# Kernel optimization log

Hardware: AMD Instinct MI355X
Metric: run time of the kernel (lower is better)

Reference implementation:

```python
import jax, jax.numpy as jnp
import numpy as np

T, B, I, H, LBL = 200, 1024, 128, 128, 4


def setup_inputs() -> dict:
    key = jax.random.key(0)
    ks = jax.random.split(key, 14)
    si = 1.0 / np.sqrt(I)
    sh = 1.0 / np.sqrt(H)
    inputs = jax.random.normal(ks[0], (T, B, I), jnp.float32)
    lengths = jnp.maximum(jax.random.randint(ks[1], (B,), 1, T + 1), LBL).astype(jnp.int32)
    return {
        "inputs": inputs,
        "lengths": lengths,
        "Wih_g": jax.random.normal(ks[2], (3 * H, I), jnp.float32) * si,
        "Whh_g": jax.random.normal(ks[3], (3 * H, H), jnp.float32) * sh,
        "bih_g": jax.random.normal(ks[4], (3 * H,), jnp.float32) * sh,
        "bhh_g": jax.random.normal(ks[5], (3 * H,), jnp.float32) * sh,
        "Wih_l": jax.random.normal(ks[6], (3 * H, I), jnp.float32) * si,
        "Whh_l": jax.random.normal(ks[7], (3 * H, H), jnp.float32) * sh,
        "bih_l": jax.random.normal(ks[8], (3 * H,), jnp.float32) * sh,
        "bhh_l": jax.random.normal(ks[9], (3 * H,), jnp.float32) * sh,
        "A1": jax.random.normal(ks[10], (H, H), jnp.float32) * sh,
        "A2": jax.random.normal(ks[11], (H, H), jnp.float32) * sh,
        "v1": jax.random.normal(ks[12], (1, H), jnp.float32) * sh,
        "label_len": LBL,
    }


def gru(x, Wih, Whh, bih, bhh):
    # x: [T, B, I] time-major. PyTorch GRU cell semantics.
    Bq, Hq = x.shape[1], Whh.shape[1]
    gi_all = jnp.einsum('tbi,gi->tbg', x, Wih) + bih  # precompute input projections [T,B,3H]
    def step(h, gi):
        gh = h @ Whh.T + bhh
        ir, iz, inn = jnp.split(gi, 3, axis=-1)
        hr, hz, hn = jnp.split(gh, 3, axis=-1)
        r = jax.nn.sigmoid(ir + hr)
        z = jax.nn.sigmoid(iz + hz)
        n = jnp.tanh(inn + r * hn)
        h = (1.0 - z) * n + z * h
        return h, h
    h0 = jnp.zeros((Bq, Hq), x.dtype)
    _, hs = jax.lax.scan(step, h0, gi_all)
    return hs  # [T, B, H]


def reference(inputs, lengths, Wih_g, Whh_g, bih_g, bhh_g,
              Wih_l, Whh_l, bih_l, bhh_l, A1, A2, v1, label_len):
    h_g = gru(inputs, Wih_g, Whh_g, bih_g, bhh_g)  # [T,B,H]
    h_l = gru(inputs, Wih_l, Whh_l, bih_l, bhh_l)  # [T,B,H]
    # attention score per step s: v1(sigmoid(A1 h_l + A2 h_g)), query-independent
    pre = jax.nn.sigmoid(jnp.einsum('tbh,gh->tbg', h_l, A1) +
                         jnp.einsum('tbh,gh->tbg', h_g, A2))
    scores = jnp.einsum('tbg,og->tbo', pre, v1)  # [T,B,1]
    # per-t output = cumsum_{s<=t}(score*h_l) + h_g[t]
    out = jnp.cumsum(scores * h_l, axis=0) + h_g  # [T,B,H]
    out_b = jnp.transpose(out, (1, 0, 2))  # [B,T,H]
    # gather last label_len timesteps of each sequence: h[b,k] = out[L_b-label_len+k, b]
    idx = lengths[:, None].astype(jnp.int32) - label_len + jnp.arange(label_len, dtype=jnp.int32)[None, :]
    idx = jnp.clip(idx, 0, out_b.shape[1] - 1)  # [B, label_len]
    h = jnp.take_along_axis(out_b, idx[:, :, None], axis=1)  # [B, label_len, H]
    return h
```

## Files before the change

### kernel.cpp

```cpp
#include <hip/hip_runtime.h>
#include <stdint.h>


typedef __attribute__((ext_vector_type(8))) short short8;
typedef __attribute__((ext_vector_type(4))) float float4v;

#define LDS_BARRIER() asm volatile("s_waitcnt lgkmcnt(0)\n\ts_barrier" ::: "memory")

__device__ inline float bf2f(unsigned short u){
  union { unsigned int i; float f; } v; v.i = ((unsigned int)u) << 16; return v.f;
}
__device__ inline unsigned short f2bf(float f){
  union { float f; unsigned int i; } v; v.f = f;
  unsigned int x = v.i;
  return (unsigned short)((x + 0x7fffu + ((x >> 16) & 1u)) >> 16);
}
__device__ inline unsigned int pack2(float a, float b){
  return (unsigned int)f2bf(a) | ((unsigned int)f2bf(b) << 16);
}
__device__ inline float sigm(float x){ return __builtin_amdgcn_rcpf(1.0f + __expf(-x)); }
__device__ inline float tanhfast(float x){ return 1.0f - 2.0f * __builtin_amdgcn_rcpf(__expf(2.0f * x) + 1.0f); }

__global__ void k_prep(unsigned short* hl_slot, unsigned short* hg_slot, float* cum)
{
  int i = blockIdx.x * blockDim.x + threadIdx.x;
  hl_slot[i] = 0;
  hg_slot[i] = 0;
  cum[i] = 0.0f;
}

__global__ __launch_bounds__(512, 2) void k_scan(
    const float* __restrict__ x,
    const float* __restrict__ Wih_g, const float* __restrict__ Whh_g,
    const float* __restrict__ bih_g, const float* __restrict__ bhh_g,
    const float* __restrict__ Wih_l, const float* __restrict__ Whh_l,
    const float* __restrict__ bih_l, const float* __restrict__ bhh_l,
    unsigned short* __restrict__ hl_seq, unsigned short* __restrict__ hg_seq,
    int tc, int t0)
{
  __shared__ __align__(16) unsigned short hbuf[2][16][136];
  __shared__ __align__(16) unsigned short xbuf[2][16][136];
  int tid = threadIdx.x;
  int w = tid >> 6, L = tid & 63, l15 = L & 15, q = L >> 4;
  int gru = blockIdx.x & 1;
  int b0 = (blockIdx.x >> 1) * 16;
  const float* Wih = gru ? Wih_l : Wih_g;
  const float* Whh = gru ? Whh_l : Whh_g;
  const float* bih = gru ? bih_l : bih_g;
  const float* bhh = gru ? bhh_l : bhh_g;
  unsigned short* myseq = gru ? hl_seq : hg_seq;

  int col = w * 16 + l15;

  short8 Wi[3][4], Wh[3][4];
  #pragma unroll
  for (int G = 0; G < 3; G++) {
    int row = G * 128 + col;
    #pragma unroll
    for (int kf = 0; kf < 4; kf++) {
      const float4* p0 = (const float4*)(Wih + (size_t)row * 128 + kf * 32 + q * 8);
      const float4* p1 = (const float4*)(Whh + (size_t)row * 128 + kf * 32 + q * 8);
      float4 a0 = p0[0], a1 = p0[1], b0f = p1[0], b1f = p1[1];
      short8 si, sh;
      si[0]=(short)f2bf(a0.x); si[1]=(short)f2bf(a0.y); si[2]=(short)f2bf(a0.z); si[3]=(short)f2bf(a0.w);
      si[4]=(short)f2bf(a1.x); si[5]=(short)f2bf(a1.y); si[6]=(short)f2bf(a1.z); si[7]=(short)f2bf(a1.w);
      sh[0]=(short)f2bf(b0f.x); sh[1]=(short)f2bf(b0f.y); sh[2]=(short)f2bf(b0f.z); sh[3]=(short)f2bf(b0f.w);
      sh[4]=(short)f2bf(b1f.x); sh[5]=(short)f2bf(b1f.y); sh[6]=(short)f2bf(b1f.z); sh[7]=(short)f2bf(b1f.w);
      Wi[G][kf] = si; Wh[G][kf] = sh;
    }
  }
  float br  = bih[col]       + bhh[col];
  float bz  = bih[128 + col] + bhh[128 + col];
  float bin = bih[256 + col];
  float bnh = bhh[256 + col];

  float hold[4];
  #pragma unroll
  for (int r = 0; r < 4; r++) {
    int m = q * 4 + r;
    unsigned short u = myseq[((size_t)(tc - 1) * 1024 + b0 + m) * 128 + col];
    hold[r] = bf2f(u);
    hbuf[0][m][col] = u;
  }
  {
    float4 x0 = ((const float4*)(x + ((size_t)t0 * 1024 + b0) * 128))[tid];
    int row = tid >> 5, c4 = (tid & 31) * 4;
    *(uint2*)&xbuf[0][row][c4] = make_uint2(pack2(x0.x, x0.y), pack2(x0.z, x0.w));
  }
  int tn = t0 + (tc > 1 ? 1 : 0);
  float4 xr = ((const float4*)(x + ((size_t)tn * 1024 + b0) * 128))[tid];
  __syncthreads();

  int p = 0;
  for (int s = 0; s < tc; s++) {
    short8 Ah[4], Ax[4];
    #pragma unroll
    for (int kf = 0; kf < 4; kf++) {
      Ah[kf] = *(const short8*)&hbuf[p][l15][kf * 32 + q * 8];
      Ax[kf] = *(const short8*)&xbuf[p][l15][kf * 32 + q * 8];
    }
    if (s + 1 < tc) {
      int row = tid >> 5, c4 = (tid & 31) * 4;
      *(uint2*)&xbuf[1 - p][row][c4] = make_uint2(pack2(xr.x, xr.y), pack2(xr.z, xr.w));
    }
    {
      int t2 = t0 + (s + 2 < tc ? s + 2 : tc - 1);
      xr = ((const float4*)(x + ((size_t)t2 * 1024 + b0) * 128))[tid];
    }
    float4v arz0 = (float4v){0.f,0.f,0.f,0.f};
    float4v arz1 = (float4v){0.f,0.f,0.f,0.f};
    float4v anx  = (float4v){0.f,0.f,0.f,0.f};
    float4v anh  = (float4v){0.f,0.f,0.f,0.f};
    #pragma unroll
    for (int kf = 0; kf < 4; kf++) arz0 = __builtin_amdgcn_mfma_f32_16x16x32_bf16(Ax[kf], Wi[0][kf], arz0, 0,0,0);
    #pragma unroll
    for (int kf = 0; kf < 4; kf++) arz1 = __builtin_amdgcn_mfma_f32_16x16x32_bf16(Ax[kf], Wi[1][kf], arz1, 0,0,0);
    #pragma unroll
    for (int kf = 0; kf < 4; kf++) anx  = __builtin_amdgcn_mfma_f32_16x16x32_bf16(Ax[kf], Wi[2][kf], anx,  0,0,0);
    #pragma unroll
    for (int kf = 0; kf < 4; kf++) anh  = __builtin_amdgcn_mfma_f32_16x16x32_bf16(Ah[kf], Wh[2][kf], anh,  0,0,0);
    #pragma unroll
    for (int kf = 0; kf < 4; kf++) arz0 = __builtin_amdgcn_mfma_f32_16x16x32_bf16(Ah[kf], Wh[0][kf], arz0, 0,0,0);
    #pragma unroll
    for (int kf = 0; kf < 4; kf++) arz1 = __builtin_amdgcn_mfma_f32_16x16x32_bf16(Ah[kf], Wh[1][kf], arz1, 0,0,0);

    #pragma unroll
    for (int r = 0; r < 4; r++) {
      int m = q * 4 + r;
      float rr = sigm(arz0[r] + br);
      float zz = sigm(arz1[r] + bz);
      float nn = tanhfast(anx[r] + bin + rr * (anh[r] + bnh));
      float hn = nn + zz * (hold[r] - nn);
      hold[r] = hn;
      unsigned short hu = f2bf(hn);
      hbuf[1 - p][m][col] = hu;
      myseq[((size_t)s * 1024 + b0 + m) * 128 + col] = hu;
    }
    p ^= 1;
    LDS_BARRIER();
  }
}

__global__ __launch_bounds__(256) void k_score(const unsigned short* __restrict__ hl_seq,
                                               const unsigned short* __restrict__ hg_seq,
                                               const float* __restrict__ A1,
                                               const float* __restrict__ A2,
                                               const float* __restrict__ v1,
                                               float* __restrict__ score, int tc)
{
  __shared__ __align__(16) unsigned short M1[128][136];
  __shared__ __align__(16) unsigned short M2[128][136];
  int tid = threadIdx.x;
  int w = tid >> 6, L = tid & 63;
  int l15 = L & 15, q = L >> 4;
  int s = blockIdx.x;

  #pragma unroll
  for (int it = 0; it < 16; it++) {
    int f4 = it * 256 + tid;
    float4 a = ((const float4*)A1)[f4];
    float4 b = ((const float4*)A2)[f4];
    *(uint2*)&M1[f4 >> 5][(f4 & 31) * 4] = make_uint2(pack2(a.x, a.y), pack2(a.z, a.w));
    *(uint2*)&M2[f4 >> 5][(f4 & 31) * 4] = make_uint2(pack2(b.x, b.y), pack2(b.z, b.w));
  }
  __syncthreads();

  float v1v[8];
  #pragma unroll
  for (int nt = 0; nt < 8; nt++) v1v[nt] = v1[nt * 16 + l15];

  short8 Fl[4], Fg[4], Pl[4], Pg[4];
  {
    size_t base = ((size_t)s * 1024 + (size_t)w * 16 + l15) * 128;
    #pragma unroll
    for (int kf = 0; kf < 4; kf++) {
      Fl[kf] = *(const short8*)(hl_seq + base + kf * 32 + q * 8);
      Fg[kf] = *(const short8*)(hg_seq + base + kf * 32 + q * 8);
    }
  }
  for (int it = 0; it < 16; it++) {
    int b0 = (it * 4 + w) * 16;
    if (it + 1 < 16) {
      size_t base = ((size_t)s * 1024 + (size_t)((it + 1) * 4 + w) * 16 + l15) * 128;
      #pragma unroll
      for (int kf = 0; kf < 4; kf++) {
        Pl[kf] = *(const short8*)(hl_seq + base + kf * 32 + q * 8);
        Pg[kf] = *(const short8*)(hg_seq + base + kf * 32 + q * 8);
      }
    }
    float4v acc[8];
    #pragma unroll
    for (int nt = 0; nt < 8; nt++) {
      float4v a = (float4v){0.f, 0.f, 0.f, 0.f};
      #pragma unroll
      for (int kf = 0; kf < 4; kf++)
        a = __builtin_amdgcn_mfma_f32_16x16x32_bf16(
            Fl[kf], *(const short8*)&M1[nt * 16 + l15][kf * 32 + q * 8], a, 0, 0, 0);
      #pragma unroll
      for (int kf = 0; kf < 4; kf++)
        a = __builtin_amdgcn_mfma_f32_16x16x32_bf16(
            Fg[kf], *(const short8*)&M2[nt * 16 + l15][kf * 32 + q * 8], a, 0, 0, 0);
      acc[nt] = a;
    }
    float p4[4];
    #pragma unroll
    for (int r = 0; r < 4; r++) {
      float sum = 0.f;
      #pragma unroll
      for (int nt = 0; nt < 8; nt++) sum += v1v[nt] * sigm(acc[nt][r]);
      sum += __shfl_xor(sum, 1, 16);
      sum += __shfl_xor(sum, 2, 16);
      sum += __shfl_xor(sum, 4, 16);
      sum += __shfl_xor(sum, 8, 16);
      p4[r] = sum;
    }
    if (l15 == 0) {
      #pragma unroll
      for (int r = 0; r < 4; r++)
        score[(size_t)(b0 + q * 4 + r) * tc + s] = p4[r];
    }
    #pragma unroll
    for (int kf = 0; kf < 4; kf++) { Fl[kf] = Pl[kf]; Fg[kf] = Pg[kf]; }
  }
}

__global__ __launch_bounds__(256) void k_cum(const float* __restrict__ score,
                                             const unsigned short* __restrict__ hl_seq,
                                             const unsigned short* __restrict__ hg_seq,
                                             const int* __restrict__ lengths,
                                             float* __restrict__ cum,
                                             float* __restrict__ out, int tc, int t0)
{
  __shared__ __align__(16) unsigned short hlL[100 * 256];
  __shared__ float scL[2][100];
  int tid = threadIdx.x;
  int b2 = tid >> 7, j = tid & 127;
  int b0 = blockIdx.x * 2;
  int b = b0 + b2;
  int base = b2 * 128 + j;

  float c = cum[(size_t)b * 128 + j];
  int cap0 = lengths[b] - 4;

  float hgv[4];
  #pragma unroll
  for (int d = 0; d < 4; d++) {
    int sl = cap0 + d - t0;
    hgv[d] = (sl >= 0 && sl < tc) ? bf2f(hg_seq[((size_t)sl * 1024 + b) * 128 + j]) : 0.f;
  }

  for (int seg = 0; seg < tc; seg += 100) {
    int len = (tc - seg < 100) ? (tc - seg) : 100;
    __syncthreads();
    for (int f8 = tid; f8 < len * 32; f8 += 256) {
      int sl = f8 >> 5, r8 = f8 & 31;
      *(short8*)&hlL[(size_t)f8 * 8] =
          *(const short8*)(hl_seq + ((size_t)(seg + sl) * 1024 + b0) * 128 + r8 * 8);
    }
    for (int i = tid; i < 2 * len; i += 256) {
      int bb = (i >= len) ? 1 : 0;
      int sl = i - bb * len;
      scL[bb][sl] = score[(size_t)(b0 + bb) * tc + seg + sl];
    }
    __syncthreads();

    int sl = 0;
    for (; sl + 5 <= len; sl += 5) {
      float h[5], sc[5];
      #pragma unroll
      for (int k = 0; k < 5; k++) {
        h[k] = bf2f(hlL[(size_t)(sl + k) * 256 + base]);
        sc[k] = scL[b2][sl + k];
      }
      #pragma unroll
      for (int k = 0; k < 5; k++) {
        c += sc[k] * h[k];
        int d = (t0 + seg + sl + k) - cap0;
        if ((unsigned)d < 4u)
          out[((size_t)b * 4 + d) * 128 + j] = c + hgv[d];
      }
    }
    for (; sl < len; sl++) {
      c += scL[b2][sl] * bf2f(hlL[(size_t)sl * 256 + base]);
      int d = (t0 + seg + sl) - cap0;
      if ((unsigned)d < 4u)
        out[((size_t)b * 4 + d) * 128 + j] = c + hgv[d];
    }
  }
  cum[(size_t)b * 128 + j] = c;
}

extern "C" void kernel_launch(void* const* d_in, const int* in_sizes, int n_in,
                              void* d_out, int out_size, void* d_ws, size_t ws_size,
                              hipStream_t stream)
{
  const float* x     = (const float*)d_in[0];
  const int* lengths = (const int*)d_in[1];
  const float* Wih_g = (const float*)d_in[2];
  const float* Whh_g = (const float*)d_in[3];
  const float* bih_g = (const float*)d_in[4];
  const float* bhh_g = (const float*)d_in[5];
  const float* Wih_l = (const float*)d_in[6];
  const float* Whh_l = (const float*)d_in[7];
  const float* bih_l = (const float*)d_in[8];
  const float* bhh_l = (const float*)d_in[9];
  const float* A1    = (const float*)d_in[10];
  const float* A2    = (const float*)d_in[11];
  const float* v1    = (const float*)d_in[12];
  float* out = (float*)d_out;

  const int cands[8] = {200, 100, 50, 25, 10, 5, 2, 1};
  int tc = 0;
  for (int i = 0; i < 8; i++) {
    int T = cands[i];
    size_t need = 2 * (size_t)T * 1024 * 128 * 2
                + (size_t)T * 1024 * 4
                + 524288;
    if (need <= ws_size) { tc = T; break; }
  }
  if (!tc) return;

  char* wsb = (char*)d_ws;
  size_t o = 0;
  unsigned short* hl  = (unsigned short*)(wsb + o); o += (size_t)tc * 1024 * 128 * 2;
  unsigned short* hg  = (unsigned short*)(wsb + o); o += (size_t)tc * 1024 * 128 * 2;
  float* score = (float*)(wsb + o); o += (size_t)tc * 1024 * 4;
  float* cum   = (float*)(wsb + o);

  unsigned short* hl_slot = hl + (size_t)(tc - 1) * 1024 * 128;
  unsigned short* hg_slot = hg + (size_t)(tc - 1) * 1024 * 128;

  k_prep<<<512, 256, 0, stream>>>(hl_slot, hg_slot, cum);
  int nch = 200 / tc;
  for (int c = 0; c < nch; c++) {
    k_scan<<<128, 512, 0, stream>>>(x, Wih_g, Whh_g, bih_g, bhh_g,
                                    Wih_l, Whh_l, bih_l, bhh_l, hl, hg, tc, c * tc);
    k_score<<<tc, 256, 0, stream>>>(hl, hg, A1, A2, v1, score, tc);
    k_cum<<<512, 256, 0, stream>>>(score, hl, hg, lengths, cum, out, tc, c * tc);
  }
}
```

Baseline: 438.1 us.

## Unroll GRU scan by two, share reciprocal in gates, split score kernel across batch

The scan loop becomes a lambda called twice per iteration, so the LDS ping-pong buffer indices are compile-time constants. The gate math now uses one reciprocal for both sigmoids and a simpler output pointer increment, with separate accumulators for the input and hidden MFMA chains. The attention weights A1/A2 are converted to bf16 once in the prep kernel, so each score block loads ready-made bf16 instead of converting fp32 on every launch. The score kernel grid is split in two across the batch with 512 threads per block, giving twice as many blocks. The costs are more register pressure from the six accumulators and the unroll, plus a changed workspace layout.

```diff
diff --git a/kernel.cpp b/kernel.cpp
--- a/kernel.cpp
+++ b/kernel.cpp
@@ -19,14 +19,17 @@
   return (unsigned int)f2bf(a) | ((unsigned int)f2bf(b) << 16);
 }
 __device__ inline float sigm(float x){ return __builtin_amdgcn_rcpf(1.0f + __expf(-x)); }
-__device__ inline float tanhfast(float x){ return 1.0f - 2.0f * __builtin_amdgcn_rcpf(__expf(2.0f * x) + 1.0f); }
-
-__global__ void k_prep(unsigned short* hl_slot, unsigned short* hg_slot, float* cum)
+
+__global__ void k_prep(unsigned short* hl_slot, unsigned short* hg_slot, float* cum,
+                       const float* A1, const float* A2, unsigned short* a12)
 {
   int i = blockIdx.x * blockDim.x + threadIdx.x;
   hl_slot[i] = 0;
   hg_slot[i] = 0;
   cum[i] = 0.0f;
+  if (i < 32768) {
+    a12[i] = f2bf((i < 16384) ? A1[i] : A2[i - 16384]);
+  }
 }
 
 __global__ __launch_bounds__(512, 2) void k_scan(
@@ -82,69 +85,78 @@
     hold[r] = bf2f(u);
     hbuf[0][m][col] = u;
   }
+  int xrow = tid >> 5, xc4 = (tid & 31) * 4;
   {
     float4 x0 = ((const float4*)(x + ((size_t)t0 * 1024 + b0) * 128))[tid];
-    int row = tid >> 5, c4 = (tid & 31) * 4;
-    *(uint2*)&xbuf[0][row][c4] = make_uint2(pack2(x0.x, x0.y), pack2(x0.z, x0.w));
+    *(uint2*)&xbuf[0][xrow][xc4] = make_uint2(pack2(x0.x, x0.y), pack2(x0.z, x0.w));
   }
   int tn = t0 + (tc > 1 ? 1 : 0);
   float4 xr = ((const float4*)(x + ((size_t)tn * 1024 + b0) * 128))[tid];
   __syncthreads();
 
-  int p = 0;
-  for (int s = 0; s < tc; s++) {
-    short8 Ah[4], Ax[4];
-    #pragma unroll
-    for (int kf = 0; kf < 4; kf++) {
-      Ah[kf] = *(const short8*)&hbuf[p][l15][kf * 32 + q * 8];
-      Ax[kf] = *(const short8*)&xbuf[p][l15][kf * 32 + q * 8];
-    }
-    if (s + 1 < tc) {
-      int row = tid >> 5, c4 = (tid & 31) * 4;
-      *(uint2*)&xbuf[1 - p][row][c4] = make_uint2(pack2(xr.x, xr.y), pack2(xr.z, xr.w));
-    }
+  unsigned short* opq = myseq + ((size_t)(b0 + q * 4)) * 128 + col;
+
+  auto step = [&](int s, int pin, int pout) {
+    short8 Ax[4], Ah[4];
+    #pragma unroll
+    for (int kf = 0; kf < 4; kf++) Ax[kf] = *(const short8*)&xbuf[pin][l15][kf * 32 + q * 8];
+    #pragma unroll
+    for (int kf = 0; kf < 4; kf++) Ah[kf] = *(const short8*)&hbuf[pin][l15][kf * 32 + q * 8];
+
+    *(uint2*)&xbuf[pout][xrow][xc4] = make_uint2(pack2(xr.x, xr.y), pack2(xr.z, xr.w));
     {
       int t2 = t0 + (s + 2 < tc ? s + 2 : tc - 1);
       xr = ((const float4*)(x + ((size_t)t2 * 1024 + b0) * 128))[tid];
     }
-    float4v arz0 = (float4v){0.f,0.f,0.f,0.f};
-    float4v arz1 = (float4v){0.f,0.f,0.f,0.f};
-    float4v anx  = (float4v){0.f,0.f,0.f,0.f};
-    float4v anh  = (float4v){0.f,0.f,0.f,0.f};
-    #pragma unroll
-    for (int kf = 0; kf < 4; kf++) arz0 = __builtin_amdgcn_mfma_f32_16x16x32_bf16(Ax[kf], Wi[0][kf], arz0, 0,0,0);
-    #pragma unroll
-    for (int kf = 0; kf < 4; kf++) arz1 = __builtin_amdgcn_mfma_f32_16x16x32_bf16(Ax[kf], Wi[1][kf], arz1, 0,0,0);
-    #pragma unroll
-    for (int kf = 0; kf < 4; kf++) anx  = __builtin_amdgcn_mfma_f32_16x16x32_bf16(Ax[kf], Wi[2][kf], anx,  0,0,0);
-    #pragma unroll
-    for (int kf = 0; kf < 4; kf++) anh  = __builtin_amdgcn_mfma_f32_16x16x32_bf16(Ah[kf], Wh[2][kf], anh,  0,0,0);
-    #pragma unroll
-    for (int kf = 0; kf < 4; kf++) arz0 = __builtin_amdgcn_mfma_f32_16x16x32_bf16(Ah[kf], Wh[0][kf], arz0, 0,0,0);
-    #pragma unroll
-    for (int kf = 0; kf < 4; kf++) arz1 = __builtin_amdgcn_mfma_f32_16x16x32_bf16(Ah[kf], Wh[1][kf], arz1, 0,0,0);
+
+    float4v rx = (float4v){0.f,0.f,0.f,0.f}, zx = rx, nx = rx;
+    float4v rh = rx, zh = rx, nh = rx;
+    #pragma unroll
+    for (int kf = 0; kf < 4; kf++) rx = __builtin_amdgcn_mfma_f32_16x16x32_bf16(Ax[kf], Wi[0][kf], rx, 0,0,0);
+    #pragma unroll
+    for (int kf = 0; kf < 4; kf++) zx = __builtin_amdgcn_mfma_f32_16x16x32_bf16(Ax[kf], Wi[1][kf], zx, 0,0,0);
+    #pragma unroll
+    for (int kf = 0; kf < 4; kf++) nx = __builtin_amdgcn_mfma_f32_16x16x32_bf16(Ax[kf], Wi[2][kf], nx, 0,0,0);
+    #pragma unroll
+    for (int kf = 0; kf < 4; kf++) rh = __builtin_amdgcn_mfma_f32_16x16x32_bf16(Ah[kf], Wh[0][kf], rh, 0,0,0);
+    #pragma unroll
+    for (int kf = 0; kf < 4; kf++) zh = __builtin_amdgcn_mfma_f32_16x16x32_bf16(Ah[kf], Wh[1][kf], zh, 0,0,0);
+    #pragma unroll
+    for (int kf = 0; kf < 4; kf++) nh = __builtin_amdgcn_mfma_f32_16x16x32_bf16(Ah[kf], Wh[2][kf], nh, 0,0,0);
+
+    float cr[4], cz[4], cn[4];
+    #pragma unroll
+    for (int r = 0; r < 4; r++) { cr[r] = rx[r] + br; cz[r] = zx[r] + bz; cn[r] = nx[r] + bin; }
 
     #pragma unroll
     for (int r = 0; r < 4; r++) {
-      int m = q * 4 + r;
-      float rr = sigm(arz0[r] + br);
-      float zz = sigm(arz1[r] + bz);
-      float nn = tanhfast(anx[r] + bin + rr * (anh[r] + bnh));
+      float er = __expf(-(rh[r] + cr[r]));
+      float ez = __expf(-(zh[r] + cz[r]));
+      float pr = 1.0f + er, pz = 1.0f + ez;
+      float inv = __builtin_amdgcn_rcpf(pr * pz);
+      float rr = pz * inv;
+      float zz = pr * inv;
+      float y  = cn[r] + rr * (nh[r] + bnh);
+      float em = __expf(-2.0f * y);
+      float nn = 2.0f * __builtin_amdgcn_rcpf(1.0f + em) - 1.0f;
       float hn = nn + zz * (hold[r] - nn);
       hold[r] = hn;
       unsigned short hu = f2bf(hn);
-      hbuf[1 - p][m][col] = hu;
-      myseq[((size_t)s * 1024 + b0 + m) * 128 + col] = hu;
-    }
-    p ^= 1;
+      hbuf[pout][q * 4 + r][col] = hu;
+      opq[r * 128] = hu;
+    }
+    opq += 131072;
     LDS_BARRIER();
-  }
-}
-
-__global__ __launch_bounds__(256) void k_score(const unsigned short* __restrict__ hl_seq,
+  };
+
+  int s = 0;
+  for (; s + 1 < tc; s += 2) { step(s, 0, 1); step(s + 1, 1, 0); }
+  if (s < tc) step(s, 0, 1);
+}
+
+__global__ __launch_bounds__(512) void k_score(const unsigned short* __restrict__ hl_seq,
                                                const unsigned short* __restrict__ hg_seq,
-                                               const float* __restrict__ A1,
-                                               const float* __restrict__ A2,
+                                               const unsigned short* __restrict__ a12,
                                                const float* __restrict__ v1,
                                                float* __restrict__ score, int tc)
 {
@@ -154,14 +166,13 @@
   int w = tid >> 6, L = tid & 63;
   int l15 = L & 15, q = L >> 4;
   int s = blockIdx.x;
-
-  #pragma unroll
-  for (int it = 0; it < 16; it++) {
-    int f4 = it * 256 + tid;
-    float4 a = ((const float4*)A1)[f4];
-    float4 b = ((const float4*)A2)[f4];
-    *(uint2*)&M1[f4 >> 5][(f4 & 31) * 4] = make_uint2(pack2(a.x, a.y), pack2(a.z, a.w));
-    *(uint2*)&M2[f4 >> 5][(f4 & 31) * 4] = make_uint2(pack2(b.x, b.y), pack2(b.z, b.w));
+  int bhalf = blockIdx.y * 512;
+
+  #pragma unroll
+  for (int it = 0; it < 4; it++) {
+    int f8 = it * 512 + tid;
+    *(short8*)&M1[f8 >> 4][(f8 & 15) * 8] = *(const short8*)(a12 + (size_t)f8 * 8);
+    *(short8*)&M2[f8 >> 4][(f8 & 15) * 8] = *(const short8*)(a12 + 16384 + (size_t)f8 * 8);
   }
   __syncthreads();
 
@@ -171,17 +182,18 @@
 
   short8 Fl[4], Fg[4], Pl[4], Pg[4];
   {
-    size_t base = ((size_t)s * 1024 + (size_t)w * 16 + l15) * 128;
+    size_t base = ((size_t)s * 1024 + bhalf + (size_t)w * 16 + l15) * 128;
     #pragma unroll
     for (int kf = 0; kf < 4; kf++) {
       Fl[kf] = *(const short8*)(hl_seq + base + kf * 32 + q * 8);
       Fg[kf] = *(const short8*)(hg_seq + base + kf * 32 + q * 8);
     }
   }
-  for (int it = 0; it < 16; it++) {
-    int b0 = (it * 4 + w) * 16;
-    if (it + 1 < 16) {
-      size_t base = ((size_t)s * 1024 + (size_t)((it + 1) * 4 + w) * 16 + l15) * 128;
+  #pragma unroll
+  for (int it = 0; it < 4; it++) {
+    int b0 = bhalf + (it * 8 + w) * 16;
+    if (it + 1 < 4) {
+      size_t base = ((size_t)s * 1024 + bhalf + (size_t)((it + 1) * 8 + w) * 16 + l15) * 128;
       #pragma unroll
       for (int kf = 0; kf < 4; kf++) {
         Pl[kf] = *(const short8*)(hl_seq + base + kf * 32 + q * 8);
@@ -309,33 +321,35 @@
   const float* v1    = (const float*)d_in[12];
   float* out = (float*)d_out;
 
-  const int cands[8] = {200, 100, 50, 25, 10, 5, 2, 1};
+  const size_t fixed = 65536 + 524288;
+  const int cands[7] = {200, 100, 50, 10, 4, 2, 1};
   int tc = 0;
-  for (int i = 0; i < 8; i++) {
+  for (int i = 0; i < 7; i++) {
     int T = cands[i];
     size_t need = 2 * (size_t)T * 1024 * 128 * 2
                 + (size_t)T * 1024 * 4
-                + 524288;
+                + fixed;
     if (need <= ws_size) { tc = T; break; }
   }
   if (!tc) return;
 
   char* wsb = (char*)d_ws;
   size_t o = 0;
+  unsigned short* a12 = (unsigned short*)(wsb + o); o += 65536;
+  float* cum   = (float*)(wsb + o); o += 524288;
   unsigned short* hl  = (unsigned short*)(wsb + o); o += (size_t)tc * 1024 * 128 * 2;
   unsigned short* hg  = (unsigned short*)(wsb + o); o += (size_t)tc * 1024 * 128 * 2;
-  float* score = (float*)(wsb + o); o += (size_t)tc * 1024 * 4;
-  float* cum   = (float*)(wsb + o);
+  float* score = (float*)(wsb + o);
 
   unsigned short* hl_slot = hl + (size_t)(tc - 1) * 1024 * 128;
   unsigned short* hg_slot = hg + (size_t)(tc - 1) * 1024 * 128;
 
-  k_prep<<<512, 256, 0, stream>>>(hl_slot, hg_slot, cum);
+  k_prep<<<512, 256, 0, stream>>>(hl_slot, hg_slot, cum, A1, A2, a12);
   int nch = 200 / tc;
   for (int c = 0; c < nch; c++) {
     k_scan<<<128, 512, 0, stream>>>(x, Wih_g, Whh_g, bih_g, bhh_g,
                                     Wih_l, Whh_l, bih_l, bhh_l, hl, hg, tc, c * tc);
-    k_score<<<tc, 256, 0, stream>>>(hl, hg, A1, A2, v1, score, tc);
+    k_score<<<dim3(tc, 2), 512, 0, stream>>>(hl, hg, a12, v1, score, tc);
     k_cum<<<512, 256, 0, stream>>>(score, hl, hg, lengths, cum, out, tc, c * tc);
   }
 }
```

After: 402.1 us. 8.2% less time.
